# Optimization experiments

Hardware: AMD Instinct MI355X
Metric: run time of the kernel (lower is better)

The kernel has to match this reference:

```python
import jax, jax.numpy as jnp
import numpy as np

NUM_HEADS = 16


def setup_inputs() -> dict:
    key = jax.random.key(0)
    k1, k2, k3 = jax.random.split(key, 3)
    B, N, C = 8, 1024, 1024
    z_k = jax.random.normal(k1, (B, N, C), dtype=jnp.float32)
    x = jax.random.normal(k2, (B, N, C), dtype=jnp.float32)
    # orthogonal-ish init for qkv weight (faithful scale to nn.init.orthogonal_)
    W = jax.random.normal(k3, (3 * C, C), dtype=jnp.float32)
    q_mat, _ = jnp.linalg.qr(W.T)  # [C, C] not full 3C rank; tile for full weight
    Wqkv = jnp.concatenate([q_mat.T, q_mat.T, q_mat.T], axis=0)  # [3C, C]
    bqkv = jnp.zeros((3 * C,), dtype=jnp.float32)
    temperature = jnp.ones((NUM_HEADS,), dtype=jnp.float32)
    return {"z_k": z_k, "x": x, "Wqkv": Wqkv, "bqkv": bqkv, "temperature": temperature}


def reference(z_k, x, Wqkv, bqkv, temperature):
    B, N, C = z_k.shape
    H = NUM_HEADS
    D = C // H
    # fused QKV projection; v from the projection is discarded (v comes from x)
    qkv = (z_k @ Wqkv.T + bqkv).reshape(B, N, 3, H, D)
    q = qkv[:, :, 0]  # [B, N, H, D]
    k = qkv[:, :, 1]  # [B, N, H, D]
    scale = D ** (-0.5)
    attn = jnp.einsum("bnhd,bmhd->bhnm", q, k) * scale  # [B, H, N, N]
    attn = attn / temperature[None, :, None, None]
    causal_mask = jnp.triu(jnp.ones((N, N), dtype=bool), k=1)
    attn = jnp.where(causal_mask[None, None], -jnp.inf, attn)
    attn = jax.nn.softmax(attn, axis=-1)
    v = x.reshape(B, N, H, D)
    z_next = jnp.einsum("bhnm,bmhd->bnhd", attn, v).reshape(B, N, C)
    return jnp.tanh(z_next)
```

## Files before the change

kernel.cpp:

```cpp
#include <hip/hip_runtime.h>
#include <hip/hip_bf16.h>

typedef __bf16 bf16_t;
typedef __bf16 bf16x4 __attribute__((ext_vector_type(4)));
typedef __bf16 bf16x8 __attribute__((ext_vector_type(8)));
typedef float  f32x4  __attribute__((ext_vector_type(4)));

#define NB 8
#define NN 1024
#define NC 1024
#define NH 16
#define ND 64
#define NBH 128
#define LOG2E 1.44269504088896340736f

__device__ __forceinline__ void gload_lds16(const bf16_t* g, bf16_t* l) {
  __builtin_amdgcn_global_load_lds(
      (const __attribute__((address_space(1))) void*)g,
      (__attribute__((address_space(3))) void*)l, 16, 0, 0);
}

__global__ void cast_f32_bf16_k(const float* __restrict__ src, bf16_t* __restrict__ dst) {
  size_t i = ((size_t)blockIdx.x * blockDim.x + threadIdx.x) * 8;
  float4 f0 = *(const float4*)(src + i);
  float4 f1 = *(const float4*)(src + i + 4);
  bf16x8 o;
  o[0]=(bf16_t)f0.x; o[1]=(bf16_t)f0.y; o[2]=(bf16_t)f0.z; o[3]=(bf16_t)f0.w;
  o[4]=(bf16_t)f1.x; o[5]=(bf16_t)f1.y; o[6]=(bf16_t)f1.z; o[7]=(bf16_t)f1.w;
  *(bf16x8*)(dst + i) = o;
}

__global__ void build_vt_k(const float* __restrict__ x, bf16_t* __restrict__ vt) {
  const int j = blockIdx.x, bh = blockIdx.y;
  const int b = bh >> 4, h = bh & 15;
  __shared__ bf16_t T[64][65];
  const int t = threadIdx.x;
  {
    const int mm = t >> 2, ds = (t & 3) * 16;
    const float* src = x + ((size_t)((b << 10) + (j << 6) + mm)) * NC + (h << 6) + ds;
    #pragma unroll
    for (int e = 0; e < 16; e += 4) {
      float4 f = *(const float4*)(src + e);
      T[mm][ds + e + 0] = (bf16_t)f.x;
      T[mm][ds + e + 1] = (bf16_t)f.y;
      T[mm][ds + e + 2] = (bf16_t)f.z;
      T[mm][ds + e + 3] = (bf16_t)f.w;
    }
  }
  __syncthreads();
  {
    const int d = t >> 2, ms = (t & 3) * 16;
    bf16_t* dstp = vt + (size_t)bh * (ND * NN) + (size_t)d * NN + (j << 6) + ms;
    bf16x8 o0, o1;
    #pragma unroll
    for (int e = 0; e < 8; ++e) { o0[e] = T[ms + e][d]; o1[e] = T[ms + 8 + e][d]; }
    *(bf16x8*)(dstp) = o0;
    *(bf16x8*)(dstp + 8) = o1;
  }
}

__global__ __launch_bounds__(256) void gemm_qk_k(
    const bf16_t* __restrict__ A, const bf16_t* __restrict__ Bw,
    const float* __restrict__ bias, const float* __restrict__ temp,
    bf16_t* __restrict__ Qg, bf16_t* __restrict__ Kg) {
  __shared__ bf16_t As[128 * 32];
  __shared__ bf16_t Bs[128 * 32];
  const int bid = blockIdx.x;
  const int xcd = bid & 7, cc = bid >> 3;
  const int by = xcd * 8 + (cc >> 3), bx = cc & 7;
  const int rowBase = by * 128;
  const int colBase = bx * 128;
  const int tid = threadIdx.x;
  const int w = tid >> 6, lane = tid & 63;
  const int wr = w >> 1, wc = w & 1;
  const int il = lane & 15, g = lane >> 4;
  const int cs = ((g ^ ((il >> 1) & 3)) << 4);

  f32x4 acc[4][4];
  #pragma unroll
  for (int i = 0; i < 4; ++i)
    #pragma unroll
    for (int j = 0; j < 4; ++j) acc[i][j] = (f32x4){0.f, 0.f, 0.f, 0.f};

  const char* Ab = (const char*)As;
  const char* Bb = (const char*)Bs;

  for (int k0 = 0; k0 < 1024; k0 += 32) {
    __syncthreads();
    #pragma unroll
    for (int inst = 0; inst < 2; ++inst) {
      const int u = inst * 256 + w * 64 + lane;
      const int row = u >> 2;
      const int kb = (((u & 3) ^ ((u >> 3) & 3)) * 8);
      gload_lds16(A  + (size_t)(rowBase + row) * 1024 + k0 + kb, &As[u * 8]);
      gload_lds16(Bw + (size_t)(colBase + row) * 1024 + k0 + kb, &Bs[u * 8]);
    }
    __syncthreads();
    bf16x8 a[4], bb[4];
    #pragma unroll
    for (int i = 0; i < 4; ++i) a[i]  = *(const bf16x8*)(Ab + (wr * 64 + i * 16 + il) * 64 + cs);
    #pragma unroll
    for (int j = 0; j < 4; ++j) bb[j] = *(const bf16x8*)(Bb + (wc * 64 + j * 16 + il) * 64 + cs);
    #pragma unroll
    for (int i = 0; i < 4; ++i)
      #pragma unroll
      for (int j = 0; j < 4; ++j)
        acc[i][j] = __builtin_amdgcn_mfma_f32_16x16x32_bf16(a[i], bb[j], acc[i][j], 0, 0, 0);
  }

  #pragma unroll
  for (int i = 0; i < 4; ++i) {
    const int mbase = rowBase + wr * 64 + i * 16 + g * 4;
    #pragma unroll
    for (int j = 0; j < 4; ++j) {
      const int n = colBase + wc * 64 + j * 16 + il;
      const int h = n >> 6, d = n & 63;
      const float bq = bias[n], bk = bias[1024 + n];
      const float qs = 0.125f * LOG2E / temp[h];
      #pragma unroll
      for (int r = 0; r < 4; ++r) {
        const int mg = mbase + r;
        const int brow = mg >> 10, nrow = mg & 1023;
        const float raw = acc[i][j][r];
        const size_t idx = (((size_t)(brow * 16 + h)) * 1024 + nrow) * 64 + d;
        Qg[idx] = (bf16_t)((raw + bq) * qs);
        Kg[idx] = (bf16_t)(raw + bk);
      }
    }
  }
}

__global__ __launch_bounds__(256) void flash_attn_k(
    const bf16_t* __restrict__ Qg, const bf16_t* __restrict__ Kg,
    const bf16_t* __restrict__ Vt, float* __restrict__ out) {
  const int idx = blockIdx.x;
  const int bh = idx & 127;
  const int qb = 15 - (idx >> 7);
  const int b = bh >> 4, h = bh & 15;
  __shared__ bf16_t Pl[4 * 16 * 64];
  __shared__ bf16_t Ks[2][64 * 64];
  __shared__ bf16_t Vts[2][64 * 64];
  const int tid = threadIdx.x, w = tid >> 6, lane = tid & 63;
  const int il = lane & 15, g = lane >> 4;
  const int sw = (il & 7) << 4;

  const int qrow_loc = w * 16 + il;
  const int qrow = qb * 64 + qrow_loc;
  const bf16_t* qptr = Qg + ((size_t)bh * 1024 + qrow) * 64;
  bf16x8 qf0 = *(const bf16x8*)(qptr + 8 * g);
  bf16x8 qf1 = *(const bf16x8*)(qptr + 32 + 8 * g);

  const size_t kbase = (size_t)bh * 1024 * 64;
  const size_t vbase = (size_t)bh * (ND * NN);

  auto stage = [&](int j, int buf) {
    #pragma unroll
    for (int inst = 0; inst < 2; ++inst) {
      const int u = inst * 256 + tid;
      const int row = u >> 3, c = (u & 7) ^ (row & 7);
      gload_lds16(Kg + kbase + ((size_t)(j * 64 + row)) * 64 + c * 8, &Ks[buf][u * 8]);
      gload_lds16(Vt + vbase + (size_t)row * NN + j * 64 + c * 8, &Vts[buf][u * 8]);
    }
  };

  stage(0, 0);
  asm volatile("s_waitcnt vmcnt(0)" ::: "memory");
  __builtin_amdgcn_s_barrier();
  asm volatile("" ::: "memory");
  if (qb >= 1) stage(1, 1);

  float l_run = 0.f;
  f32x4 acc[4];
  #pragma unroll
  for (int td = 0; td < 4; ++td) acc[td] = (f32x4){0.f, 0.f, 0.f, 0.f};

  char* Pb = (char*)Pl + w * 2048;

  for (int j = 0; j <= qb; ++j) {
    const int cur = j & 1;
    const char* Kb = (const char*)Ks[cur];
    const char* Vb = (const char*)Vts[cur];

    f32x4 s[4];
    __builtin_amdgcn_s_setprio(1);
    #pragma unroll
    for (int t = 0; t < 4; ++t) {
      const int krow = t * 16 + il;
      bf16x8 k0 = *(const bf16x8*)(Kb + krow * 128 + ((16 * g) ^ sw));
      bf16x8 k1 = *(const bf16x8*)(Kb + krow * 128 + ((64 + 16 * g) ^ sw));
      s[t] = (f32x4){0.f, 0.f, 0.f, 0.f};
      s[t] = __builtin_amdgcn_mfma_f32_16x16x32_bf16(k0, qf0, s[t], 0, 0, 0);
      s[t] = __builtin_amdgcn_mfma_f32_16x16x32_bf16(k1, qf1, s[t], 0, 0, 0);
    }
    __builtin_amdgcn_s_setprio(0);

    #pragma unroll
    for (int t = 0; t < 4; ++t) {
      float p0, p1, p2, p3;
      if (j == qb) {
        const int kg = j * 64 + t * 16 + g * 4;
        p0 = (kg + 0 > qrow) ? 0.f : exp2f(s[t][0]);
        p1 = (kg + 1 > qrow) ? 0.f : exp2f(s[t][1]);
        p2 = (kg + 2 > qrow) ? 0.f : exp2f(s[t][2]);
        p3 = (kg + 3 > qrow) ? 0.f : exp2f(s[t][3]);
      } else {
        p0 = exp2f(s[t][0]); p1 = exp2f(s[t][1]);
        p2 = exp2f(s[t][2]); p3 = exp2f(s[t][3]);
      }
      l_run += (p0 + p1) + (p2 + p3);
      bf16x4 pk;
      pk[0] = (bf16_t)p0; pk[1] = (bf16_t)p1; pk[2] = (bf16_t)p2; pk[3] = (bf16_t)p3;
      *(bf16x4*)(Pb + il * 128 + ((t * 32 + g * 8) ^ sw)) = pk;
    }

    bf16x8 pf0 = *(const bf16x8*)(Pb + il * 128 + ((16 * g) ^ sw));
    bf16x8 pf1 = *(const bf16x8*)(Pb + il * 128 + ((64 + 16 * g) ^ sw));
    __builtin_amdgcn_s_setprio(1);
    #pragma unroll
    for (int td = 0; td < 4; ++td) {
      const int drow = td * 16 + il;
      bf16x8 v0 = *(const bf16x8*)(Vb + drow * 128 + ((16 * g) ^ sw));
      bf16x8 v1 = *(const bf16x8*)(Vb + drow * 128 + ((64 + 16 * g) ^ sw));
      acc[td] = __builtin_amdgcn_mfma_f32_16x16x32_bf16(v0, pf0, acc[td], 0, 0, 0);
      acc[td] = __builtin_amdgcn_mfma_f32_16x16x32_bf16(v1, pf1, acc[td], 0, 0, 0);
    }
    __builtin_amdgcn_s_setprio(0);

    if (j < qb) {
      asm volatile("s_waitcnt vmcnt(0)" ::: "memory");
      __builtin_amdgcn_s_barrier();
      asm volatile("" ::: "memory");
      if (j + 2 <= qb) stage(j + 2, cur);
    }
  }

  l_run += __shfl_xor(l_run, 16, 64);
  l_run += __shfl_xor(l_run, 32, 64);
  const float inv = 1.0f / l_run;
  float* orow = out + ((size_t)b * 1024 + qrow) * 1024 + (h << 6);
  #pragma unroll
  for (int td = 0; td < 4; ++td) {
    float4 o;
    o.x = tanhf(acc[td][0] * inv);
    o.y = tanhf(acc[td][1] * inv);
    o.z = tanhf(acc[td][2] * inv);
    o.w = tanhf(acc[td][3] * inv);
    *(float4*)(orow + td * 16 + g * 4) = o;
  }
}

extern "C" void kernel_launch(void* const* d_in, const int* in_sizes, int n_in,
                              void* d_out, int out_size, void* d_ws, size_t ws_size,
                              hipStream_t stream) {
  const float* z_k  = (const float*)d_in[0];
  const float* x    = (const float*)d_in[1];
  const float* Wqkv = (const float*)d_in[2];
  const float* bqkv = (const float*)d_in[3];
  const float* temp = (const float*)d_in[4];
  float* out = (float*)d_out;

  char* ws = (char*)d_ws;
  bf16_t* A  = (bf16_t*)(ws);
  bf16_t* Bw = (bf16_t*)(ws + 16777216);
  bf16_t* Qg = (bf16_t*)(ws + 16777216 + 4194304);
  bf16_t* Kg = (bf16_t*)(ws + 16777216 + 4194304 + 16777216);
  bf16_t* Vt = (bf16_t*)(ws + 16777216 + 4194304 + 2 * 16777216);

  cast_f32_bf16_k<<<4096, 256, 0, stream>>>(z_k, A);
  cast_f32_bf16_k<<<512, 256, 0, stream>>>(Wqkv, Bw);
  build_vt_k<<<dim3(16, 128), 256, 0, stream>>>(x, Vt);
  gemm_qk_k<<<512, 256, 0, stream>>>(A, Bw, bqkv, temp, Qg, Kg);
  flash_attn_k<<<2048, 256, 0, stream>>>(Qg, Kg, Vt, out);
}
```

Before: 93.09 us.

## Split attention work across waves by key rows, keeping P in registers

Each wave now owns 16 key rows of every KV tile and all 64 query rows, instead of 16 query rows. The probability tile is passed straight from the QK MFMA output into 16x16x16 MFMAs as the B operand, which removes the per-iteration LDS round trip for P. Partial outputs and row sums from the four waves are reduced through LDS in the epilogue. In exchange it holds 16 accumulator tiles per thread, adds several barriers in the epilogue, and uses MFMAs with half the K depth, which raises register pressure and may lower occupancy.

```diff
diff --git a/kernel.cpp b/kernel.cpp
--- a/kernel.cpp
+++ b/kernel.cpp
@@ -5,6 +5,7 @@
 typedef __bf16 bf16x4 __attribute__((ext_vector_type(4)));
 typedef __bf16 bf16x8 __attribute__((ext_vector_type(8)));
 typedef float  f32x4  __attribute__((ext_vector_type(4)));
+typedef short  short4_ __attribute__((ext_vector_type(4)));
 
 #define NB 8
 #define NN 1024
@@ -18,6 +19,21 @@
   __builtin_amdgcn_global_load_lds(
       (const __attribute__((address_space(1))) void*)g,
       (__attribute__((address_space(3))) void*)l, 16, 0, 0);
+}
+
+__device__ __forceinline__ f32x4 mfma16(bf16x4 a, bf16x4 b, f32x4 c) {
+#if __has_builtin(__builtin_amdgcn_mfma_f32_16x16x16bf16_1k)
+  return __builtin_amdgcn_mfma_f32_16x16x16bf16_1k(
+      __builtin_bit_cast(short4_, a), __builtin_bit_cast(short4_, b), c, 0, 0, 0);
+#elif __has_builtin(__builtin_amdgcn_mfma_f32_16x16x16_bf16)
+  return __builtin_amdgcn_mfma_f32_16x16x16_bf16(a, b, c, 0, 0, 0);
+#else
+  asm volatile("s_nop 1\n\t"
+               "v_mfma_f32_16x16x16_bf16 %0, %1, %2, %0\n\t"
+               "s_nop 7\n\ts_nop 3"
+               : "+v"(c) : "v"(a), "v"(b));
+  return c;
+#endif
 }
 
 __global__ void cast_f32_bf16_k(const float* __restrict__ src, bf16_t* __restrict__ dst) {
@@ -137,18 +153,22 @@
   const int bh = idx & 127;
   const int qb = 15 - (idx >> 7);
   const int b = bh >> 4, h = bh & 15;
-  __shared__ bf16_t Pl[4 * 16 * 64];
   __shared__ bf16_t Ks[2][64 * 64];
   __shared__ bf16_t Vts[2][64 * 64];
   const int tid = threadIdx.x, w = tid >> 6, lane = tid & 63;
   const int il = lane & 15, g = lane >> 4;
-  const int sw = (il & 7) << 4;
-
-  const int qrow_loc = w * 16 + il;
-  const int qrow = qb * 64 + qrow_loc;
-  const bf16_t* qptr = Qg + ((size_t)bh * 1024 + qrow) * 64;
-  bf16x8 qf0 = *(const bf16x8*)(qptr + 8 * g);
-  bf16x8 qf1 = *(const bf16x8*)(qptr + 32 + 8 * g);
+  const int sw7 = il & 7;
+
+  bf16x8 qf[4][2];
+  {
+    const bf16_t* qbase = Qg + ((size_t)bh * 1024 + qb * 64) * 64;
+    #pragma unroll
+    for (int t = 0; t < 4; ++t) {
+      const bf16_t* qp = qbase + (size_t)(t * 16 + il) * 64 + 8 * g;
+      qf[t][0] = *(const bf16x8*)(qp);
+      qf[t][1] = *(const bf16x8*)(qp + 32);
+    }
+  }
 
   const size_t kbase = (size_t)bh * 1024 * 64;
   const size_t vbase = (size_t)bh * (ND * NN);
@@ -169,60 +189,58 @@
   asm volatile("" ::: "memory");
   if (qb >= 1) stage(1, 1);
 
-  float l_run = 0.f;
-  f32x4 acc[4];
-  #pragma unroll
-  for (int td = 0; td < 4; ++td) acc[td] = (f32x4){0.f, 0.f, 0.f, 0.f};
-
-  char* Pb = (char*)Pl + w * 2048;
+  float lp[4] = {0.f, 0.f, 0.f, 0.f};
+  f32x4 acc[4][4];
+  #pragma unroll
+  for (int t = 0; t < 4; ++t)
+    #pragma unroll
+    for (int td = 0; td < 4; ++td) acc[t][td] = (f32x4){0.f, 0.f, 0.f, 0.f};
+
+  const int krow_lds = w * 16 + il;
 
   for (int j = 0; j <= qb; ++j) {
     const int cur = j & 1;
     const char* Kb = (const char*)Ks[cur];
     const char* Vb = (const char*)Vts[cur];
 
+    bf16x8 k0 = *(const bf16x8*)(Kb + krow_lds * 128 + ((g ^ sw7) << 4));
+    bf16x8 k1 = *(const bf16x8*)(Kb + krow_lds * 128 + (((4 + g) ^ sw7) << 4));
+
     f32x4 s[4];
     __builtin_amdgcn_s_setprio(1);
     #pragma unroll
     for (int t = 0; t < 4; ++t) {
-      const int krow = t * 16 + il;
-      bf16x8 k0 = *(const bf16x8*)(Kb + krow * 128 + ((16 * g) ^ sw));
-      bf16x8 k1 = *(const bf16x8*)(Kb + krow * 128 + ((64 + 16 * g) ^ sw));
       s[t] = (f32x4){0.f, 0.f, 0.f, 0.f};
-      s[t] = __builtin_amdgcn_mfma_f32_16x16x32_bf16(k0, qf0, s[t], 0, 0, 0);
-      s[t] = __builtin_amdgcn_mfma_f32_16x16x32_bf16(k1, qf1, s[t], 0, 0, 0);
+      s[t] = __builtin_amdgcn_mfma_f32_16x16x32_bf16(k0, qf[t][0], s[t], 0, 0, 0);
+      s[t] = __builtin_amdgcn_mfma_f32_16x16x32_bf16(k1, qf[t][1], s[t], 0, 0, 0);
     }
     __builtin_amdgcn_s_setprio(0);
 
+    bf16x4 pb[4];
+    const bool diag = (j == qb);
+    const int kloc = w * 16 + g * 4;
     #pragma unroll
     for (int t = 0; t < 4; ++t) {
-      float p0, p1, p2, p3;
-      if (j == qb) {
-        const int kg = j * 64 + t * 16 + g * 4;
-        p0 = (kg + 0 > qrow) ? 0.f : exp2f(s[t][0]);
-        p1 = (kg + 1 > qrow) ? 0.f : exp2f(s[t][1]);
-        p2 = (kg + 2 > qrow) ? 0.f : exp2f(s[t][2]);
-        p3 = (kg + 3 > qrow) ? 0.f : exp2f(s[t][3]);
-      } else {
-        p0 = exp2f(s[t][0]); p1 = exp2f(s[t][1]);
-        p2 = exp2f(s[t][2]); p3 = exp2f(s[t][3]);
-      }
-      l_run += (p0 + p1) + (p2 + p3);
+      const int qloc = t * 16 + il;
+      float p0 = (diag && kloc + 0 > qloc) ? 0.f : exp2f(s[t][0]);
+      float p1 = (diag && kloc + 1 > qloc) ? 0.f : exp2f(s[t][1]);
+      float p2 = (diag && kloc + 2 > qloc) ? 0.f : exp2f(s[t][2]);
+      float p3 = (diag && kloc + 3 > qloc) ? 0.f : exp2f(s[t][3]);
+      lp[t] += (p0 + p1) + (p2 + p3);
       bf16x4 pk;
       pk[0] = (bf16_t)p0; pk[1] = (bf16_t)p1; pk[2] = (bf16_t)p2; pk[3] = (bf16_t)p3;
-      *(bf16x4*)(Pb + il * 128 + ((t * 32 + g * 8) ^ sw)) = pk;
-    }
-
-    bf16x8 pf0 = *(const bf16x8*)(Pb + il * 128 + ((16 * g) ^ sw));
-    bf16x8 pf1 = *(const bf16x8*)(Pb + il * 128 + ((64 + 16 * g) ^ sw));
+      pb[t] = pk;
+    }
+
     __builtin_amdgcn_s_setprio(1);
     #pragma unroll
     for (int td = 0; td < 4; ++td) {
-      const int drow = td * 16 + il;
-      bf16x8 v0 = *(const bf16x8*)(Vb + drow * 128 + ((16 * g) ^ sw));
-      bf16x8 v1 = *(const bf16x8*)(Vb + drow * 128 + ((64 + 16 * g) ^ sw));
-      acc[td] = __builtin_amdgcn_mfma_f32_16x16x32_bf16(v0, pf0, acc[td], 0, 0, 0);
-      acc[td] = __builtin_amdgcn_mfma_f32_16x16x32_bf16(v1, pf1, acc[td], 0, 0, 0);
+      const int vrow = td * 16 + il;
+      bf16x4 va = *(const bf16x4*)(Vb + vrow * 128 +
+                    ((((w * 2) + (g >> 1)) ^ sw7) << 4) + ((g & 1) << 3));
+      #pragma unroll
+      for (int t = 0; t < 4; ++t)
+        acc[t][td] = mfma16(va, pb[t], acc[t][td]);
     }
     __builtin_amdgcn_s_setprio(0);
 
@@ -234,18 +252,49 @@
     }
   }
 
-  l_run += __shfl_xor(l_run, 16, 64);
-  l_run += __shfl_xor(l_run, 32, 64);
-  const float inv = 1.0f / l_run;
-  float* orow = out + ((size_t)b * 1024 + qrow) * 1024 + (h << 6);
+  asm volatile("s_waitcnt vmcnt(0) lgkmcnt(0)" ::: "memory");
+  __builtin_amdgcn_s_barrier();
+  asm volatile("" ::: "memory");
+
+  float* lbuf = (float*)&Ks[0][0];
+  float* Rbuf = (float*)&Vts[0][0];
+  #pragma unroll
+  for (int t = 0; t < 4; ++t) {
+    float v = lp[t];
+    v += __shfl_xor(v, 16, 64);
+    v += __shfl_xor(v, 32, 64);
+    if (g == 0) lbuf[(w * 4 + t) * 16 + il] = v;
+  }
+  #pragma unroll
+  for (int t = 0; t < 4; ++t)
+    *(f32x4*)(Rbuf + ((w * 4 + t) * 64 + il * 4 + g) * 4) = acc[t][0];
+  __syncthreads();
+
+  const int q = tid >> 2, tt = q >> 4, ril = q & 15, dseg = tid & 3;
+  float lsum = lbuf[(0 * 4 + tt) * 16 + ril] + lbuf[(1 * 4 + tt) * 16 + ril] +
+               lbuf[(2 * 4 + tt) * 16 + ril] + lbuf[(3 * 4 + tt) * 16 + ril];
+  const float inv = 1.0f / lsum;
+  float* orow = out + ((size_t)b * 1024 + qb * 64 + q) * 1024 + (h << 6);
+
   #pragma unroll
   for (int td = 0; td < 4; ++td) {
-    float4 o;
-    o.x = tanhf(acc[td][0] * inv);
-    o.y = tanhf(acc[td][1] * inv);
-    o.z = tanhf(acc[td][2] * inv);
-    o.w = tanhf(acc[td][3] * inv);
-    *(float4*)(orow + td * 16 + g * 4) = o;
+    if (td) {
+      __syncthreads();
+      #pragma unroll
+      for (int t = 0; t < 4; ++t)
+        *(f32x4*)(Rbuf + ((w * 4 + t) * 64 + il * 4 + g) * 4) = acc[t][td];
+      __syncthreads();
+    }
+    f32x4 o = (f32x4){0.f, 0.f, 0.f, 0.f};
+    #pragma unroll
+    for (int ww = 0; ww < 4; ++ww)
+      o += *(const f32x4*)(Rbuf + ((ww * 4 + tt) * 64 + ril * 4 + dseg) * 4);
+    float4 ov;
+    ov.x = tanhf(o[0] * inv);
+    ov.y = tanhf(o[1] * inv);
+    ov.z = tanhf(o[2] * inv);
+    ov.w = tanhf(o[3] * inv);
+    *(float4*)(orow + td * 16 + dseg * 4) = ov;
   }
 }
 
```

Result: slower. 119.1 us (+28.0%).

## Compute softmax row sums via MFMA, use fast exp/rcp/tanh, unroll loop by two

Applied to the files above, without the earlier changes.

The attention kernel now gets the softmax denominator from an extra MFMA against a ones vector instead of scalar adds and cross-lane shuffles. It also replaces exp2f, division and tanhf with hardware v_exp/v_rcp intrinsics and a rcp-based tanh. The tile loop is unrolled by two so the double-buffer index is a compile-time constant. The row sum is now taken over the bf16-rounded probabilities, and the fast tanh can overflow to inf for large inputs, though it still saturates correctly.

```diff
diff --git a/kernel.cpp b/kernel.cpp
--- a/kernel.cpp
+++ b/kernel.cpp
@@ -18,6 +18,31 @@
   __builtin_amdgcn_global_load_lds(
       (const __attribute__((address_space(1))) void*)g,
       (__attribute__((address_space(3))) void*)l, 16, 0, 0);
+}
+
+__device__ __forceinline__ float fast_exp2(float x) {
+#if __has_builtin(__builtin_amdgcn_exp2f)
+  return __builtin_amdgcn_exp2f(x);
+#else
+  float r;
+  asm volatile("v_exp_f32 %0, %1\n\ts_nop 0" : "=v"(r) : "v"(x));
+  return r;
+#endif
+}
+
+__device__ __forceinline__ float fast_rcp(float x) {
+#if __has_builtin(__builtin_amdgcn_rcpf)
+  return __builtin_amdgcn_rcpf(x);
+#else
+  float r;
+  asm volatile("v_rcp_f32 %0, %1\n\ts_nop 0" : "=v"(r) : "v"(x));
+  return r;
+#endif
+}
+
+__device__ __forceinline__ float fast_tanh(float z) {
+  float e = fast_exp2(z * (2.0f * LOG2E));
+  return 1.0f - 2.0f * fast_rcp(e + 1.0f);
 }
 
 __global__ void cast_f32_bf16_k(const float* __restrict__ src, bf16_t* __restrict__ dst) {
@@ -150,6 +175,10 @@
   bf16x8 qf0 = *(const bf16x8*)(qptr + 8 * g);
   bf16x8 qf1 = *(const bf16x8*)(qptr + 32 + 8 * g);
 
+  bf16x8 ones;
+  #pragma unroll
+  for (int e = 0; e < 8; ++e) ones[e] = (bf16_t)1.0f;
+
   const size_t kbase = (size_t)bh * 1024 * 64;
   const size_t vbase = (size_t)bh * (ND * NN);
 
@@ -163,89 +192,94 @@
     }
   };
 
+  const int nt = qb + 1;
   stage(0, 0);
   asm volatile("s_waitcnt vmcnt(0)" ::: "memory");
   __builtin_amdgcn_s_barrier();
   asm volatile("" ::: "memory");
-  if (qb >= 1) stage(1, 1);
-
-  float l_run = 0.f;
+  if (nt > 1) stage(1, 1);
+
   f32x4 acc[4];
+  f32x4 acc_l;
   #pragma unroll
   for (int td = 0; td < 4; ++td) acc[td] = (f32x4){0.f, 0.f, 0.f, 0.f};
+  acc_l = (f32x4){0.f, 0.f, 0.f, 0.f};
 
   char* Pb = (char*)Pl + w * 2048;
 
-  for (int j = 0; j <= qb; ++j) {
-    const int cur = j & 1;
-    const char* Kb = (const char*)Ks[cur];
-    const char* Vb = (const char*)Vts[cur];
-
-    f32x4 s[4];
-    __builtin_amdgcn_s_setprio(1);
-    #pragma unroll
-    for (int t = 0; t < 4; ++t) {
-      const int krow = t * 16 + il;
-      bf16x8 k0 = *(const bf16x8*)(Kb + krow * 128 + ((16 * g) ^ sw));
-      bf16x8 k1 = *(const bf16x8*)(Kb + krow * 128 + ((64 + 16 * g) ^ sw));
-      s[t] = (f32x4){0.f, 0.f, 0.f, 0.f};
-      s[t] = __builtin_amdgcn_mfma_f32_16x16x32_bf16(k0, qf0, s[t], 0, 0, 0);
-      s[t] = __builtin_amdgcn_mfma_f32_16x16x32_bf16(k1, qf1, s[t], 0, 0, 0);
-    }
-    __builtin_amdgcn_s_setprio(0);
-
-    #pragma unroll
-    for (int t = 0; t < 4; ++t) {
-      float p0, p1, p2, p3;
-      if (j == qb) {
-        const int kg = j * 64 + t * 16 + g * 4;
-        p0 = (kg + 0 > qrow) ? 0.f : exp2f(s[t][0]);
-        p1 = (kg + 1 > qrow) ? 0.f : exp2f(s[t][1]);
-        p2 = (kg + 2 > qrow) ? 0.f : exp2f(s[t][2]);
-        p3 = (kg + 3 > qrow) ? 0.f : exp2f(s[t][3]);
-      } else {
-        p0 = exp2f(s[t][0]); p1 = exp2f(s[t][1]);
-        p2 = exp2f(s[t][2]); p3 = exp2f(s[t][3]);
-      }
-      l_run += (p0 + p1) + (p2 + p3);
-      bf16x4 pk;
-      pk[0] = (bf16_t)p0; pk[1] = (bf16_t)p1; pk[2] = (bf16_t)p2; pk[3] = (bf16_t)p3;
-      *(bf16x4*)(Pb + il * 128 + ((t * 32 + g * 8) ^ sw)) = pk;
-    }
-
-    bf16x8 pf0 = *(const bf16x8*)(Pb + il * 128 + ((16 * g) ^ sw));
-    bf16x8 pf1 = *(const bf16x8*)(Pb + il * 128 + ((64 + 16 * g) ^ sw));
-    __builtin_amdgcn_s_setprio(1);
-    #pragma unroll
-    for (int td = 0; td < 4; ++td) {
-      const int drow = td * 16 + il;
-      bf16x8 v0 = *(const bf16x8*)(Vb + drow * 128 + ((16 * g) ^ sw));
-      bf16x8 v1 = *(const bf16x8*)(Vb + drow * 128 + ((64 + 16 * g) ^ sw));
-      acc[td] = __builtin_amdgcn_mfma_f32_16x16x32_bf16(v0, pf0, acc[td], 0, 0, 0);
-      acc[td] = __builtin_amdgcn_mfma_f32_16x16x32_bf16(v1, pf1, acc[td], 0, 0, 0);
-    }
-    __builtin_amdgcn_s_setprio(0);
-
-    if (j < qb) {
-      asm volatile("s_waitcnt vmcnt(0)" ::: "memory");
-      __builtin_amdgcn_s_barrier();
-      asm volatile("" ::: "memory");
-      if (j + 2 <= qb) stage(j + 2, cur);
-    }
-  }
-
-  l_run += __shfl_xor(l_run, 16, 64);
-  l_run += __shfl_xor(l_run, 32, 64);
-  const float inv = 1.0f / l_run;
+#define TILE(J, CUR)                                                            \
+  {                                                                             \
+    const char* Kb = (const char*)Ks[CUR];                                      \
+    const char* Vb = (const char*)Vts[CUR];                                     \
+    f32x4 s[4];                                                                 \
+    __builtin_amdgcn_s_setprio(1);                                              \
+    _Pragma("unroll")                                                           \
+    for (int t = 0; t < 4; ++t) {                                               \
+      const int krow = t * 16 + il;                                             \
+      bf16x8 k0 = *(const bf16x8*)(Kb + krow * 128 + ((16 * g) ^ sw));          \
+      bf16x8 k1 = *(const bf16x8*)(Kb + krow * 128 + ((64 + 16 * g) ^ sw));     \
+      s[t] = (f32x4){0.f, 0.f, 0.f, 0.f};                                       \
+      s[t] = __builtin_amdgcn_mfma_f32_16x16x32_bf16(k0, qf0, s[t], 0, 0, 0);   \
+      s[t] = __builtin_amdgcn_mfma_f32_16x16x32_bf16(k1, qf1, s[t], 0, 0, 0);   \
+    }                                                                           \
+    __builtin_amdgcn_s_setprio(0);                                              \
+    const bool diag = ((J) == qb);                                              \
+    _Pragma("unroll")                                                           \
+    for (int t = 0; t < 4; ++t) {                                               \
+      float p0 = fast_exp2(s[t][0]);                                            \
+      float p1 = fast_exp2(s[t][1]);                                            \
+      float p2 = fast_exp2(s[t][2]);                                            \
+      float p3 = fast_exp2(s[t][3]);                                            \
+      if (diag) {                                                               \
+        const int kg = (J) * 64 + t * 16 + g * 4;                               \
+        p0 = (kg + 0 > qrow) ? 0.f : p0;                                        \
+        p1 = (kg + 1 > qrow) ? 0.f : p1;                                        \
+        p2 = (kg + 2 > qrow) ? 0.f : p2;                                        \
+        p3 = (kg + 3 > qrow) ? 0.f : p3;                                        \
+      }                                                                         \
+      bf16x4 pk;                                                                \
+      pk[0] = (bf16_t)p0; pk[1] = (bf16_t)p1;                                   \
+      pk[2] = (bf16_t)p2; pk[3] = (bf16_t)p3;                                   \
+      *(bf16x4*)(Pb + il * 128 + ((t * 32 + g * 8) ^ sw)) = pk;                 \
+    }                                                                           \
+    bf16x8 pf0 = *(const bf16x8*)(Pb + il * 128 + ((16 * g) ^ sw));             \
+    bf16x8 pf1 = *(const bf16x8*)(Pb + il * 128 + ((64 + 16 * g) ^ sw));        \
+    __builtin_amdgcn_s_setprio(1);                                              \
+    acc_l = __builtin_amdgcn_mfma_f32_16x16x32_bf16(ones, pf0, acc_l, 0, 0, 0); \
+    acc_l = __builtin_amdgcn_mfma_f32_16x16x32_bf16(ones, pf1, acc_l, 0, 0, 0); \
+    _Pragma("unroll")                                                           \
+    for (int td = 0; td < 4; ++td) {                                            \
+      const int drow = td * 16 + il;                                            \
+      bf16x8 v0 = *(const bf16x8*)(Vb + drow * 128 + ((16 * g) ^ sw));          \
+      bf16x8 v1 = *(const bf16x8*)(Vb + drow * 128 + ((64 + 16 * g) ^ sw));     \
+      acc[td] = __builtin_amdgcn_mfma_f32_16x16x32_bf16(v0, pf0, acc[td], 0, 0, 0); \
+      acc[td] = __builtin_amdgcn_mfma_f32_16x16x32_bf16(v1, pf1, acc[td], 0, 0, 0); \
+    }                                                                           \
+    __builtin_amdgcn_s_setprio(0);                                              \
+    if ((J) < nt - 1) {                                                         \
+      asm volatile("s_waitcnt vmcnt(0)" ::: "memory");                          \
+      __builtin_amdgcn_s_barrier();                                             \
+      asm volatile("" ::: "memory");                                            \
+      if ((J) + 2 < nt) stage((J) + 2, CUR);                                    \
+    }                                                                           \
+  }
+
+  for (int j0 = 0; j0 < nt; j0 += 2) {
+    TILE(j0, 0);
+    if (j0 + 1 < nt) TILE(j0 + 1, 1);
+  }
+#undef TILE
+
+  const float inv = fast_rcp(acc_l[0]);
   float* orow = out + ((size_t)b * 1024 + qrow) * 1024 + (h << 6);
   #pragma unroll
   for (int td = 0; td < 4; ++td) {
-    float4 o;
-    o.x = tanhf(acc[td][0] * inv);
-    o.y = tanhf(acc[td][1] * inv);
-    o.z = tanhf(acc[td][2] * inv);
-    o.w = tanhf(acc[td][3] * inv);
-    *(float4*)(orow + td * 16 + g * 4) = o;
+    float4 ov;
+    ov.x = fast_tanh(acc[td][0] * inv);
+    ov.y = fast_tanh(acc[td][1] * inv);
+    ov.z = fast_tanh(acc[td][2] * inv);
+    ov.w = fast_tanh(acc[td][3] * inv);
+    *(float4*)(orow + td * 16 + g * 4) = ov;
   }
 }
 
```

Result: faster. 86.85 us (-6.7%).
